# Performance work log

Measured on AMD Instinct MI355X. Metric: run time of the kernel, lower is better.

## Reference

```python
import jax, jax.numpy as jnp
import numpy as np

N_NODES = 100000
N_EDGES = 640000
D_FEAT = 128
N_HIDDEN = 32


def setup_inputs() -> dict:
    key = jax.random.key(0)
    ks = jax.random.split(key, 8)
    x = jax.random.normal(ks[0], (N_NODES, D_FEAT), dtype=jnp.float32)
    edge_index = jax.random.randint(ks[1], (2, N_EDGES), 0, N_NODES, dtype=jnp.int64)
    # Glorot-ish scaled params
    W1_l = jax.random.normal(ks[2], (D_FEAT, N_HIDDEN), dtype=jnp.float32) / np.sqrt(D_FEAT)
    W1_r = jax.random.normal(ks[3], (D_FEAT, N_HIDDEN), dtype=jnp.float32) / np.sqrt(D_FEAT)
    b1 = jnp.zeros((N_HIDDEN,), dtype=jnp.float32)
    W2_l = jax.random.normal(ks[4], (N_HIDDEN, 1), dtype=jnp.float32) / np.sqrt(N_HIDDEN)
    W2_r = jax.random.normal(ks[5], (N_HIDDEN, 1), dtype=jnp.float32) / np.sqrt(N_HIDDEN)
    b2 = jnp.zeros((1,), dtype=jnp.float32)
    return {"x": x, "edge_index": edge_index, "W1_l": W1_l, "W1_r": W1_r,
            "b1": b1, "W2_l": W2_l, "W2_r": W2_r, "b2": b2}


def _sage_conv(h, src, dst, n_nodes, W_l, W_r, b):
    # mean aggregation of source features at destination nodes (PyG SAGEConv default)
    msg_sum = jax.ops.segment_sum(h[src], dst, num_segments=n_nodes)          # [N, d]
    deg = jax.ops.segment_sum(jnp.ones_like(src, dtype=h.dtype), dst,
                              num_segments=n_nodes)                           # [N]
    mean = msg_sum / jnp.maximum(deg, 1.0)[:, None]
    return mean @ W_l + h @ W_r + b


def reference(x, edge_index, W1_l, W1_r, b1, W2_l, W2_r, b2):
    src, dst = edge_index[0], edge_index[1]
    n = x.shape[0]
    h = jax.nn.relu(_sage_conv(x, src, dst, n, W1_l, W1_r, b1))
    # dropout p=0.1 is identity at inference (training=False)
    out = _sage_conv(h, src, dst, n, W2_l, W2_r, b2)
    return out  # [N, 1] node logits
```

## Files before the change

### kernel.cpp

```cpp
#include <hip/hip_runtime.h>

#define NN 100000
#define NE 640000
#define DF 128
#define NH 32
#define CAP 32
#define BINS 1563
#define HBLK 256
#define EPB 2500
#define NTILE 6250
#define GEMMB 1563

typedef __attribute__((ext_vector_type(8))) short bf16x8;
typedef __attribute__((ext_vector_type(4))) float f32x4;

__device__ __forceinline__ unsigned short f2bf(float x) {
    union { float f; unsigned u; } c; c.f = x;
    unsigned r = c.u + 0x7fffu + ((c.u >> 16) & 1u);
    return (unsigned short)(r >> 16);
}
__device__ __forceinline__ float bf2f(unsigned short b) {
    union { unsigned u; float f; } c; c.u = ((unsigned)b) << 16;
    return c.f;
}

__global__ __launch_bounds__(256) void gemm_sort_kernel(
    const float* __restrict__ x, const float* __restrict__ W1_l,
    const float* __restrict__ W1_r, unsigned short* __restrict__ xl_bf,
    unsigned short* __restrict__ xr_bf, const int* __restrict__ src,
    const int* __restrict__ dst, int2* __restrict__ packmat,
    int* __restrict__ binned)
{
    __shared__ unsigned short wl[8192];
    __shared__ int lpart[256];

    if (blockIdx.x >= GEMMB) {
        int* lhist = (int*)wl;
        const int h = blockIdx.x - GEMMB;
        const int t = threadIdx.x;
        const int e0 = h * EPB;
        for (int b = t; b < BINS; b += 256) lhist[b] = 0;
        __syncthreads();
        for (int i = t; i < EPB; i += 256)
            atomicAdd(&lhist[dst[e0 + i] >> 6], 1);
        __syncthreads();
        const int k0 = t * 7, k1 = (k0 + 7 < BINS) ? k0 + 7 : BINS;
        int s = 0;
        for (int k = k0; k < k1; k++) s += lhist[k];
        lpart[t] = s;
        __syncthreads();
        for (int off = 1; off < 256; off <<= 1) {
            int v = (t >= off) ? lpart[t - off] : 0;
            __syncthreads();
            lpart[t] += v;
            __syncthreads();
        }
        int run = lpart[t] - s;
        for (int k = k0; k < k1; k++) {
            int c = lhist[k];
            packmat[(size_t)h * BINS + k] = make_int2(run, c);
            lhist[k] = run;
            run += c;
        }
        __syncthreads();
        for (int i = t; i < EPB; i += 256) {
            int sv = src[e0 + i], d = dst[e0 + i];
            int pos = atomicAdd(&lhist[d >> 6], 1);
            binned[e0 + pos] = (sv << 6) | (d & 63);
        }
        return;
    }

    for (int s = threadIdx.x; s < 1024; s += 256) {
        int lane = s & 63;
        int nt = (s >> 6) & 3;
        int ks = s >> 8;
        int n = nt * 16 + (lane & 15);
        const float* Wc = (n < 32) ? (W1_l + n) : (W1_r + (n - 32));
        unsigned short v[8];
#pragma unroll
        for (int i = 0; i < 8; i++) {
            int k = ks * 32 + ((i >> 2) << 4) + ((lane >> 4) << 2) + (i & 3);
            v[i] = f2bf(Wc[(size_t)k * 32]);
        }
        unsigned u0 = (unsigned)v[0] | ((unsigned)v[1] << 16);
        unsigned u1 = (unsigned)v[2] | ((unsigned)v[3] << 16);
        unsigned u2 = (unsigned)v[4] | ((unsigned)v[5] << 16);
        unsigned u3 = (unsigned)v[6] | ((unsigned)v[7] << 16);
        *(uint4*)&wl[s * 8] = make_uint4(u0, u1, u2, u3);
    }
    __syncthreads();

    const int lane = threadIdx.x & 63;
    const int tile = (blockIdx.x << 2) + (threadIdx.x >> 6);
    if (tile >= NTILE) return;
    const int m = lane & 15, g = lane >> 4;
    const int row0 = tile << 4;

#define BLOAD(ks, nt) const bf16x8 b##ks##nt = *(const bf16x8*)&wl[(((ks)*4 + (nt)) * 64 + lane) * 8];
    BLOAD(0,0) BLOAD(0,1) BLOAD(0,2) BLOAD(0,3)
    BLOAD(1,0) BLOAD(1,1) BLOAD(1,2) BLOAD(1,3)
    BLOAD(2,0) BLOAD(2,1) BLOAD(2,2) BLOAD(2,3)
    BLOAD(3,0) BLOAD(3,1) BLOAD(3,2) BLOAD(3,3)
#undef BLOAD

    f32x4 acc0 = {0.f,0.f,0.f,0.f}, acc1 = {0.f,0.f,0.f,0.f};
    f32x4 acc2 = {0.f,0.f,0.f,0.f}, acc3 = {0.f,0.f,0.f,0.f};

    const float* xp = x + (size_t)(row0 + m) * DF + g * 4;

#define KSTEP(ks) { \
    float4 fa = *(const float4*)(xp + (ks) * 32); \
    float4 fb = *(const float4*)(xp + (ks) * 32 + 16); \
    bf16x8 af; \
    af[0] = (short)f2bf(fa.x); af[1] = (short)f2bf(fa.y); \
    af[2] = (short)f2bf(fa.z); af[3] = (short)f2bf(fa.w); \
    af[4] = (short)f2bf(fb.x); af[5] = (short)f2bf(fb.y); \
    af[6] = (short)f2bf(fb.z); af[7] = (short)f2bf(fb.w); \
    acc0 = __builtin_amdgcn_mfma_f32_16x16x32_bf16(af, b##ks##0, acc0, 0, 0, 0); \
    acc1 = __builtin_amdgcn_mfma_f32_16x16x32_bf16(af, b##ks##1, acc1, 0, 0, 0); \
    acc2 = __builtin_amdgcn_mfma_f32_16x16x32_bf16(af, b##ks##2, acc2, 0, 0, 0); \
    acc3 = __builtin_amdgcn_mfma_f32_16x16x32_bf16(af, b##ks##3, acc3, 0, 0, 0); }
    KSTEP(0) KSTEP(1) KSTEP(2) KSTEP(3)
#undef KSTEP

#define CSTORE(nt) { \
    int n = (nt) * 16 + m; \
_Pragma("unroll") \
    for (int r = 0; r < 4; r++) { \
        int rr = row0 + g * 4 + r; \
        unsigned short v = f2bf(acc##nt[r]); \
        if (n < 32) xl_bf[(size_t)rr * 32 + n] = v; \
        else        xr_bf[(size_t)rr * 32 + (n - 32)] = v; \
    } }
    CSTORE(0) CSTORE(1) CSTORE(2) CSTORE(3)
#undef CSTORE
}

__global__ __launch_bounds__(256) void agg1_bin_kernel(
    const int* __restrict__ binned, const int2* __restrict__ packmat,
    const unsigned short* __restrict__ xl_bf, const unsigned short* __restrict__ xr_bf,
    const float* __restrict__ b1, const float* __restrict__ W2_l,
    const float* __restrict__ W2_r, float* __restrict__ h2l, float* __restrict__ hrp,
    int* __restrict__ esrc, int* __restrict__ deg)
{
    __shared__ int lcnt[64];
    __shared__ int lesrc[64 * CAP];
    const int j = blockIdx.x, t = threadIdx.x;
    if (t < 64) lcnt[t] = 0;
    __syncthreads();

    {
        int2 sc = packmat[(size_t)t * BINS + j];
        const int base = t * EPB + sc.x;
        for (int k = 0; k < sc.y; k++) {
            int pk = binned[base + k];
            int dl = pk & 63, s = pk >> 6;
            int p = atomicAdd(&lcnt[dl], 1);
            if (p < CAP) lesrc[(dl << 5) + p] = s;
        }
    }
    __syncthreads();

    for (int i = t; i < 64 * CAP; i += 256) {
        int node = j * 64 + (i >> 5);
        int c = lcnt[i >> 5];
        if (node < NN && (i & 31) < ((c < CAP) ? c : CAP))
            esrc[(size_t)node * CAP + (i & 31)] = lesrc[i];
    }
    if (t < 64) {
        int node = j * 64 + t;
        if (node < NN) deg[node] = lcnt[t];
    }

    const int l = t & 31, grp = t >> 5;
    const int j8 = l >> 2, c = l & 3;
    const float4* b14 = (const float4*)&b1[c * 8];
    float4 bb0 = b14[0], bb1 = b14[1];
    const float4* wl4 = (const float4*)&W2_l[c * 8];
    float4 wl0 = wl4[0], wl1 = wl4[1];
    const float4* wr4 = (const float4*)&W2_r[c * 8];
    float4 wr0 = wr4[0], wr1 = wr4[1];
    const float bs[8]  = {bb0.x, bb0.y, bb0.z, bb0.w, bb1.x, bb1.y, bb1.z, bb1.w};
    const float wls[8] = {wl0.x, wl0.y, wl0.z, wl0.w, wl1.x, wl1.y, wl1.z, wl1.w};
    const float wrs[8] = {wr0.x, wr0.y, wr0.z, wr0.w, wr1.x, wr1.y, wr1.z, wr1.w};

    for (int dl = grp; dl < 64; dl += 8) {
        const int node = j * 64 + dl;
        if (node >= NN) break;
        const int dg = lcnt[dl];
        const int lim = (dg < CAP) ? dg : CAP;

        float acc[8];
#pragma unroll
        for (int i = 0; i < 8; i++) acc[i] = 0.f;

        for (int jb = 0; jb < lim; jb += 8) {
            int jj = jb + j8;
            if (jj < lim) {
                int s = lesrc[(dl << 5) + jj];
                uint4 v = *(const uint4*)&xl_bf[(size_t)s * NH + c * 8];
#pragma unroll
                for (int i = 0; i < 4; i++) {
                    unsigned u = (&v.x)[i];
                    acc[2 * i]     += bf2f((unsigned short)(u & 0xffffu));
                    acc[2 * i + 1] += bf2f((unsigned short)(u >> 16));
                }
            }
        }
#pragma unroll
        for (int mm = 4; mm <= 16; mm <<= 1)
#pragma unroll
            for (int i = 0; i < 8; i++) acc[i] += __shfl_xor(acc[i], mm);

        const float inv = 1.0f / fmaxf((float)dg, 1.0f);
        uint4 xv = *(const uint4*)&xr_bf[(size_t)node * NH + c * 8];
        float sl = 0.f, sr = 0.f;
#pragma unroll
        for (int i = 0; i < 4; i++) {
            unsigned u = (&xv.x)[i];
            float xlo = bf2f((unsigned short)(u & 0xffffu));
            float xhi = bf2f((unsigned short)(u >> 16));
            float h0 = fmaxf(fmaf(acc[2 * i],     inv, xlo + bs[2 * i]),     0.f);
            float h1 = fmaxf(fmaf(acc[2 * i + 1], inv, xhi + bs[2 * i + 1]), 0.f);
            sl = fmaf(h0, wls[2 * i], sl); sl = fmaf(h1, wls[2 * i + 1], sl);
            sr = fmaf(h0, wrs[2 * i], sr); sr = fmaf(h1, wrs[2 * i + 1], sr);
        }
        sl += __shfl_xor(sl, 1); sl += __shfl_xor(sl, 2);
        sr += __shfl_xor(sr, 1); sr += __shfl_xor(sr, 2);
        if (l == 0) {
            h2l[node] = sl;
            hrp[node] = sr;
        }
    }
}

__global__ __launch_bounds__(256) void agg2_final_kernel(
    const int* __restrict__ deg, const int* __restrict__ esrc,
    const float* __restrict__ h2l, const float* __restrict__ hrp,
    const float* __restrict__ b2, float* __restrict__ out)
{
    int i = blockIdx.x * 256 + threadIdx.x;
    if (i >= NN) return;
    int dg = deg[i];
    int lim = (dg < CAP) ? dg : CAP;
    const int* ep = esrc + (size_t)i * CAP;
    float s0 = 0.f, s1 = 0.f, s2 = 0.f, s3 = 0.f;
    int j = 0;
    for (; j + 3 < lim; j += 4) {
        int4 s = *(const int4*)&ep[j];
        s0 += h2l[s.x];
        s1 += h2l[s.y];
        s2 += h2l[s.z];
        s3 += h2l[s.w];
    }
    for (; j < lim; j++) s0 += h2l[ep[j]];
    out[i] = ((s0 + s1) + (s2 + s3)) / fmaxf((float)dg, 1.0f) + hrp[i] + b2[0];
}

extern "C" void kernel_launch(void* const* d_in, const int* in_sizes, int n_in,
                              void* d_out, int out_size, void* d_ws, size_t ws_size,
                              hipStream_t stream)
{
    const float* x    = (const float*)d_in[0];
    const int*   ei   = (const int*)d_in[1];
    const float* W1_l = (const float*)d_in[2];
    const float* W1_r = (const float*)d_in[3];
    const float* b1   = (const float*)d_in[4];
    const float* W2_l = (const float*)d_in[5];
    const float* W2_r = (const float*)d_in[6];
    const float* b2   = (const float*)d_in[7];
    float* out = (float*)d_out;

    const int* src = ei;
    const int* dst = ei + NE;

    unsigned short* xl_bf = (unsigned short*)d_ws;
    unsigned short* xr_bf = xl_bf + (size_t)NN * NH;
    float* h2l      = (float*)(xr_bf + (size_t)NN * NH);
    float* hrp      = h2l + NN;
    int2*  packmat  = (int2*)(hrp + NN);
    int*   binned   = (int*)(packmat + (size_t)HBLK * BINS);
    int*   esrc     = binned + NE;
    int*   deg      = esrc + (size_t)NN * CAP;

    gemm_sort_kernel<<<GEMMB + HBLK, 256, 0, stream>>>(x, W1_l, W1_r, xl_bf, xr_bf,
                                                       src, dst, packmat, binned);
    agg1_bin_kernel<<<BINS, 256, 0, stream>>>(binned, packmat, xl_bf, xr_bf,
                                              b1, W2_l, W2_r, h2l, hrp, esrc, deg);
    agg2_final_kernel<<<(NN + 255) / 256, 256, 0, stream>>>(deg, esrc, h2l, hrp, b2, out);
}
```

Before: 67.06 us.

## Put sort blocks first, vectorize edge loads, double GEMM tiles per wave

Reorders the fused kernel so the histogram/sort blocks get the lowest block indices and are scheduled first, instead of trailing the GEMM blocks. Edge index reads become int4 vector loads. Each GEMM wave now processes two 16-row tiles, halving GEMM block count and amortizing the per-block weight conversion into LDS. The packmat load in the aggregation kernel is hoisted above the barrier to overlap its latency. Fewer GEMM blocks may reduce parallelism and latency hiding.

Result: faster. 63.31 us (-5.6%).

```diff
diff --git a/kernel.cpp b/kernel.cpp
--- a/kernel.cpp
+++ b/kernel.cpp
@@ -8,8 +8,9 @@
 #define BINS 1563
 #define HBLK 256
 #define EPB 2500
+#define QPB 625
 #define NTILE 6250
-#define GEMMB 1563
+#define GEMMB 782
 
 typedef __attribute__((ext_vector_type(8))) short bf16x8;
 typedef __attribute__((ext_vector_type(4))) float f32x4;
@@ -34,15 +35,22 @@
     __shared__ unsigned short wl[8192];
     __shared__ int lpart[256];
 
-    if (blockIdx.x >= GEMMB) {
+    if (blockIdx.x < HBLK) {
         int* lhist = (int*)wl;
-        const int h = blockIdx.x - GEMMB;
+        const int h = blockIdx.x;
         const int t = threadIdx.x;
         const int e0 = h * EPB;
+        const int4* dq = (const int4*)(dst + e0);
+        const int4* sq = (const int4*)(src + e0);
         for (int b = t; b < BINS; b += 256) lhist[b] = 0;
         __syncthreads();
-        for (int i = t; i < EPB; i += 256)
-            atomicAdd(&lhist[dst[e0 + i] >> 6], 1);
+        for (int q = t; q < QPB; q += 256) {
+            int4 d4 = dq[q];
+            atomicAdd(&lhist[d4.x >> 6], 1);
+            atomicAdd(&lhist[d4.y >> 6], 1);
+            atomicAdd(&lhist[d4.z >> 6], 1);
+            atomicAdd(&lhist[d4.w >> 6], 1);
+        }
         __syncthreads();
         const int k0 = t * 7, k1 = (k0 + 7 < BINS) ? k0 + 7 : BINS;
         int s = 0;
@@ -63,10 +71,15 @@
             run += c;
         }
         __syncthreads();
-        for (int i = t; i < EPB; i += 256) {
-            int sv = src[e0 + i], d = dst[e0 + i];
-            int pos = atomicAdd(&lhist[d >> 6], 1);
-            binned[e0 + pos] = (sv << 6) | (d & 63);
+        for (int q = t; q < QPB; q += 256) {
+            int4 d4 = dq[q];
+            int4 s4 = sq[q];
+#pragma unroll
+            for (int i = 0; i < 4; i++) {
+                int d = (&d4.x)[i], sv = (&s4.x)[i];
+                int pos = atomicAdd(&lhist[d >> 6], 1);
+                binned[e0 + pos] = (sv << 6) | (d & 63);
+            }
         }
         return;
     }
@@ -92,10 +105,8 @@
     __syncthreads();
 
     const int lane = threadIdx.x & 63;
-    const int tile = (blockIdx.x << 2) + (threadIdx.x >> 6);
-    if (tile >= NTILE) return;
+    const int wslot = ((blockIdx.x - HBLK) << 2) + (threadIdx.x >> 6);
     const int m = lane & 15, g = lane >> 4;
-    const int row0 = tile << 4;
 
 #define BLOAD(ks, nt) const bf16x8 b##ks##nt = *(const bf16x8*)&wl[(((ks)*4 + (nt)) * 64 + lane) * 8];
     BLOAD(0,0) BLOAD(0,1) BLOAD(0,2) BLOAD(0,3)
@@ -104,37 +115,43 @@
     BLOAD(3,0) BLOAD(3,1) BLOAD(3,2) BLOAD(3,3)
 #undef BLOAD
 
-    f32x4 acc0 = {0.f,0.f,0.f,0.f}, acc1 = {0.f,0.f,0.f,0.f};
-    f32x4 acc2 = {0.f,0.f,0.f,0.f}, acc3 = {0.f,0.f,0.f,0.f};
-
-    const float* xp = x + (size_t)(row0 + m) * DF + g * 4;
+#pragma unroll
+    for (int tt = 0; tt < 2; tt++) {
+        const int tile = wslot * 2 + tt;
+        if (tile >= NTILE) break;
+        const int row0 = tile << 4;
+        const float* xp = x + (size_t)(row0 + m) * DF + g * 4;
+
+        f32x4 acc0 = {0.f,0.f,0.f,0.f}, acc1 = {0.f,0.f,0.f,0.f};
+        f32x4 acc2 = {0.f,0.f,0.f,0.f}, acc3 = {0.f,0.f,0.f,0.f};
 
 #define KSTEP(ks) { \
-    float4 fa = *(const float4*)(xp + (ks) * 32); \
-    float4 fb = *(const float4*)(xp + (ks) * 32 + 16); \
-    bf16x8 af; \
-    af[0] = (short)f2bf(fa.x); af[1] = (short)f2bf(fa.y); \
-    af[2] = (short)f2bf(fa.z); af[3] = (short)f2bf(fa.w); \
-    af[4] = (short)f2bf(fb.x); af[5] = (short)f2bf(fb.y); \
-    af[6] = (short)f2bf(fb.z); af[7] = (short)f2bf(fb.w); \
-    acc0 = __builtin_amdgcn_mfma_f32_16x16x32_bf16(af, b##ks##0, acc0, 0, 0, 0); \
-    acc1 = __builtin_amdgcn_mfma_f32_16x16x32_bf16(af, b##ks##1, acc1, 0, 0, 0); \
-    acc2 = __builtin_amdgcn_mfma_f32_16x16x32_bf16(af, b##ks##2, acc2, 0, 0, 0); \
-    acc3 = __builtin_amdgcn_mfma_f32_16x16x32_bf16(af, b##ks##3, acc3, 0, 0, 0); }
-    KSTEP(0) KSTEP(1) KSTEP(2) KSTEP(3)
+        float4 fa = *(const float4*)(xp + (ks) * 32); \
+        float4 fb = *(const float4*)(xp + (ks) * 32 + 16); \
+        bf16x8 af; \
+        af[0] = (short)f2bf(fa.x); af[1] = (short)f2bf(fa.y); \
+        af[2] = (short)f2bf(fa.z); af[3] = (short)f2bf(fa.w); \
+        af[4] = (short)f2bf(fb.x); af[5] = (short)f2bf(fb.y); \
+        af[6] = (short)f2bf(fb.z); af[7] = (short)f2bf(fb.w); \
+        acc0 = __builtin_amdgcn_mfma_f32_16x16x32_bf16(af, b##ks##0, acc0, 0, 0, 0); \
+        acc1 = __builtin_amdgcn_mfma_f32_16x16x32_bf16(af, b##ks##1, acc1, 0, 0, 0); \
+        acc2 = __builtin_amdgcn_mfma_f32_16x16x32_bf16(af, b##ks##2, acc2, 0, 0, 0); \
+        acc3 = __builtin_amdgcn_mfma_f32_16x16x32_bf16(af, b##ks##3, acc3, 0, 0, 0); }
+        KSTEP(0) KSTEP(1) KSTEP(2) KSTEP(3)
 #undef KSTEP
 
 #define CSTORE(nt) { \
-    int n = (nt) * 16 + m; \
+        int n = (nt) * 16 + m; \
 _Pragma("unroll") \
-    for (int r = 0; r < 4; r++) { \
-        int rr = row0 + g * 4 + r; \
-        unsigned short v = f2bf(acc##nt[r]); \
-        if (n < 32) xl_bf[(size_t)rr * 32 + n] = v; \
-        else        xr_bf[(size_t)rr * 32 + (n - 32)] = v; \
-    } }
-    CSTORE(0) CSTORE(1) CSTORE(2) CSTORE(3)
+        for (int r = 0; r < 4; r++) { \
+            int rr = row0 + g * 4 + r; \
+            unsigned short v = f2bf(acc##nt[r]); \
+            if (n < 32) xl_bf[(size_t)rr * 32 + n] = v; \
+            else        xr_bf[(size_t)rr * 32 + (n - 32)] = v; \
+        } }
+        CSTORE(0) CSTORE(1) CSTORE(2) CSTORE(3)
 #undef CSTORE
+    }
 }
 
 __global__ __launch_bounds__(256) void agg1_bin_kernel(
@@ -147,11 +164,11 @@
     __shared__ int lcnt[64];
     __shared__ int lesrc[64 * CAP];
     const int j = blockIdx.x, t = threadIdx.x;
+    int2 sc = packmat[(size_t)t * BINS + j];
     if (t < 64) lcnt[t] = 0;
     __syncthreads();
 
     {
-        int2 sc = packmat[(size_t)t * BINS + j];
         const int base = t * EPB + sc.x;
         for (int k = 0; k < sc.y; k++) {
             int pk = binned[base + k];
@@ -284,7 +301,7 @@
     int*   esrc     = binned + NE;
     int*   deg      = esrc + (size_t)NN * CAP;
 
-    gemm_sort_kernel<<<GEMMB + HBLK, 256, 0, stream>>>(x, W1_l, W1_r, xl_bf, xr_bf,
+    gemm_sort_kernel<<<HBLK + GEMMB, 256, 0, stream>>>(x, W1_l, W1_r, xl_bf, xr_bf,
                                                        src, dst, packmat, binned);
     agg1_bin_kernel<<<BINS, 256, 0, stream>>>(binned, packmat, xl_bf, xr_bf,
                                               b1, W2_l, W2_r, h2l, hrp, esrc, deg);
```
